# Optimization experiments

Hardware: AMD Instinct MI355X
Metric: run time of the kernel (lower is better)

Reference implementation:

```python
import jax, jax.numpy as jnp
import numpy as np
from jax import lax

N = 7  # patch size


def _conv3d(x, w, b):
    # x: [B,1,D,H,W], w: [1,1,3,3,3], b: [1]; VALID conv, stride 1
    y = lax.conv_general_dilated(x, w, (1, 1, 1), 'VALID',
                                 dimension_numbers=('NCDHW', 'OIDHW', 'NCDHW'))
    return y + b.reshape(1, -1, 1, 1, 1)


def _patches(x, k):
    # x: [B,1,D,H,W] -> [B*D'*H'*W', 1, k, k, k], row-major (kd,kh,kw) like torch unfold
    p = lax.conv_general_dilated_patches(x, (k, k, k), (1, 1, 1), 'VALID')
    # p: [B, k^3, D', H', W'] -> [B, D', H', W', k^3]
    p = jnp.transpose(p, (0, 2, 3, 4, 1))
    return p.reshape(-1, 1, k, k, k)


def setup_inputs() -> dict:
    key = jax.random.key(0)
    ks = jax.random.split(key, 12)
    inp = {
        'x': jax.random.normal(ks[0], (1, 1, 32, 128, 128), dtype=jnp.float32),
        'domain_neighbor': jax.random.uniform(ks[1], (1, 1, 9, 9, 9), dtype=jnp.float32),
        'guide_im': jax.random.normal(ks[2], (1, 1, 32, 128, 128), dtype=jnp.float32),
        # range coefficient conv stack (2 layers of Conv3d(1,1,3))
        'rw0': jax.random.normal(ks[3], (1, 1, 3, 3, 3), dtype=jnp.float32) * 0.3,
        'rb0': jnp.full((1,), 0.1, dtype=jnp.float32),
        'rw1': jax.random.normal(ks[4], (1, 1, 3, 3, 3), dtype=jnp.float32) * 0.3,
        'rb1': jnp.full((1,), 0.1, dtype=jnp.float32),
        # domain coefficient conv stack
        'dw0': jax.random.normal(ks[5], (1, 1, 3, 3, 3), dtype=jnp.float32) * 0.3,
        'db0': jnp.full((1,), 0.1, dtype=jnp.float32),
        'dw1': jax.random.normal(ks[6], (1, 1, 3, 3, 3), dtype=jnp.float32) * 0.3,
        'db1': jnp.full((1,), 0.1, dtype=jnp.float32),
    }
    return inp


def reference(x, domain_neighbor, guide_im, rw0, rb0, rw1, rb1, dw0, db0, dw1, db1):
    n = N
    c = n // 2
    # ---- range kernel: per-patch |guide - center|, then tiny conv stack ----
    g = _patches(guide_im, n)                     # [P,1,n,n,n]
    g = jnp.abs(g - g[:, :, c, c, c][:, :, None, None, None])
    rk = jax.nn.relu(_conv3d(g, rw0, rb0))
    rk = jax.nn.relu(_conv3d(rk, rw1, rb1))       # [P,1,3,3,3]
    # ---- domain kernel: center crop of distance kernel, same conv stack ----
    M = domain_neighbor.shape[2]
    cx = M // 2 - c
    dn = domain_neighbor[:, :, cx:cx + n, cx:cx + n, cx:cx + n]  # [1,1,n,n,n]
    dk = jax.nn.relu(_conv3d(dn, dw0, db0))
    dk = jax.nn.relu(_conv3d(dk, dw1, db1))       # [1,1,3,3,3]
    weights = dk * rk + 1e-10                     # [P,1,3,3,3]
    # ---- weighted average over 3x3x3 neighborhood of truncated x ----
    p = (n - 3) // 2
    xt = x[:, :, p:x.shape[2] - p, p:x.shape[3] - p, p:x.shape[4] - p]
    xu = _patches(xt, 3)                          # [P,1,3,3,3]
    num = jnp.sum(xu * weights, axis=(2, 3, 4))   # [P,1]
    den = jnp.sum(weights, axis=(2, 3, 4))        # [P,1]
    out = num / den
    B = x.shape[0]
    return out.reshape(B, 1, x.shape[2] - n + 1, x.shape[3] - n + 1, x.shape[4] - n + 1)
```

## Files before the change

kernel.cpp:

```cpp
#include <hip/hip_runtime.h>

#define OD 26
#define OH 122
#define OW 122
#define GS (128*128)
#define NOUT (OD*OH*OW)

#define TLX 14
#define TLY 14
#define TLZ 10
#define TLSLICE (TLX*TLY)
#define TLN (TLSLICE*TLZ)

__global__ void compute_dk_kernel(const float* __restrict__ dn,
                                  const float* __restrict__ dw0, const float* __restrict__ db0,
                                  const float* __restrict__ dw1, const float* __restrict__ db1,
                                  float* __restrict__ dk_out) {
    __shared__ float d0[125];
    int t = threadIdx.x;
    if (t < 125) {
        int tz = t / 25, ty = (t / 5) % 5, tx = t % 5;
        float acc = db0[0];
        #pragma unroll
        for (int kz = 0; kz < 3; ++kz)
            #pragma unroll
            for (int ky = 0; ky < 3; ++ky)
                #pragma unroll
                for (int kx = 0; kx < 3; ++kx)
                    acc += dw0[kz*9 + ky*3 + kx] *
                           dn[(1+tz+kz)*81 + (1+ty+ky)*9 + (1+tx+kx)];
        d0[t] = fmaxf(acc, 0.0f);
    }
    __syncthreads();
    if (t < 27) {
        int rz = t / 9, ry = (t / 3) % 3, rx = t % 3;
        float acc = db1[0];
        #pragma unroll
        for (int kz = 0; kz < 3; ++kz)
            #pragma unroll
            for (int ky = 0; ky < 3; ++ky)
                #pragma unroll
                for (int kx = 0; kx < 3; ++kx)
                    acc += dw1[kz*9 + ky*3 + kx] * d0[(rz+kz)*25 + (ry+ky)*5 + (rx+kx)];
        dk_out[t] = fmaxf(acc, 0.0f);
    }
}

__global__ __launch_bounds__(256) void jbf_main_kernel(
        const float* __restrict__ x, const float* __restrict__ guide,
        const float* __restrict__ rw0p, const float* __restrict__ rb0p,
        const float* __restrict__ rw1p, const float* __restrict__ rb1p,
        const float* __restrict__ dkp, float* __restrict__ out) {
    __shared__ float gl[TLN];

    const int xb = blockIdx.x * 8;
    const int yb = blockIdx.y * 8;
    const int zb = blockIdx.z * 4;

    for (int i = threadIdx.x; i < TLN; i += 256) {
        const int gx = i % TLX;
        const int gy = (i / TLX) % TLY;
        const int gz = i / TLSLICE;
        const int sx = min(xb + gx, 127);
        const int sy = min(yb + gy, 127);
        const int sz = min(zb + gz, 31);
        gl[i] = guide[sz*GS + sy*128 + sx];
    }
    __syncthreads();

    const int tx = threadIdx.x & 7;
    const int ty = (threadIdx.x >> 3) & 7;
    const int tz = threadIdx.x >> 6;
    const int x0 = xb + tx;
    const int y0 = yb + ty;
    const int z0 = zb + tz;
    if (x0 >= OW || y0 >= OH || z0 >= OD) return;

    float rw0[27], rw1[27];
    #pragma unroll
    for (int i = 0; i < 27; ++i) { rw0[i] = rw0p[i]; rw1[i] = rw1p[i]; }
    const float rb0 = rb0p[0], rb1 = rb1p[0];

    const float* glb = &gl[tz*TLSLICE + ty*TLX + tx];
    const float gc = glb[3*TLSLICE + 3*TLX + 3];

    float t0[125];
    #pragma unroll
    for (int i = 0; i < 125; ++i) t0[i] = rb0;

    #pragma unroll
    for (int gz = 0; gz < 7; ++gz) {
        #pragma unroll
        for (int gy = 0; gy < 7; ++gy) {
            float s[7];
            #pragma unroll
            for (int j = 0; j < 7; ++j)
                s[j] = glb[gz*TLSLICE + gy*TLX + j] - gc;
            #pragma unroll
            for (int kz = 0; kz < 3; ++kz) {
                const int tz1 = gz - kz;
                if (tz1 < 0 || tz1 > 4) continue;
                #pragma unroll
                for (int ky = 0; ky < 3; ++ky) {
                    const int ty1 = gy - ky;
                    if (ty1 < 0 || ty1 > 4) continue;
                    #pragma unroll
                    for (int txx = 0; txx < 5; ++txx)
                        #pragma unroll
                        for (int kx = 0; kx < 3; ++kx)
                            t0[tz1*25 + ty1*5 + txx] =
                                fmaf(rw0[kz*9 + ky*3 + kx], fabsf(s[txx + kx]),
                                     t0[tz1*25 + ty1*5 + txx]);
                }
            }
        }
    }
    #pragma unroll
    for (int i = 0; i < 125; ++i) t0[i] = fmaxf(t0[i], 0.0f);

    float num = 0.0f, den = 0.0f;
    const float* xbp = x + (z0+2)*GS + (y0+2)*128 + (x0+2);
    #pragma unroll
    for (int rz = 0; rz < 3; ++rz)
        #pragma unroll
        for (int ry = 0; ry < 3; ++ry)
            #pragma unroll
            for (int rx = 0; rx < 3; ++rx) {
                float acc = rb1;
                #pragma unroll
                for (int kz = 0; kz < 3; ++kz)
                    #pragma unroll
                    for (int ky = 0; ky < 3; ++ky)
                        #pragma unroll
                        for (int kx = 0; kx < 3; ++kx)
                            acc = fmaf(rw1[kz*9 + ky*3 + kx],
                                       t0[(rz+kz)*25 + (ry+ky)*5 + (rx+kx)], acc);
                const float w = dkp[rz*9 + ry*3 + rx] * fmaxf(acc, 0.0f) + 1e-10f;
                den += w;
                num = fmaf(w, xbp[rz*GS + ry*128 + rx], num);
            }

    out[(z0*OH + y0)*OW + x0] = num / den;
}

extern "C" void kernel_launch(void* const* d_in, const int* in_sizes, int n_in,
                              void* d_out, int out_size, void* d_ws, size_t ws_size,
                              hipStream_t stream) {
    const float* x     = (const float*)d_in[0];
    const float* dn    = (const float*)d_in[1];
    const float* guide = (const float*)d_in[2];
    const float* rw0   = (const float*)d_in[3];
    const float* rb0   = (const float*)d_in[4];
    const float* rw1   = (const float*)d_in[5];
    const float* rb1   = (const float*)d_in[6];
    const float* dw0   = (const float*)d_in[7];
    const float* db0   = (const float*)d_in[8];
    const float* dw1   = (const float*)d_in[9];
    const float* db1   = (const float*)d_in[10];
    float* out = (float*)d_out;
    float* dk  = (float*)d_ws;

    compute_dk_kernel<<<1, 128, 0, stream>>>(dn, dw0, db0, dw1, db1, dk);

    dim3 grid((OW + 7) / 8, (OH + 7) / 8, (OD + 3) / 4);
    jbf_main_kernel<<<grid, 256, 0, stream>>>(x, guide, rw0, rb0, rw1, rb1, dk, out);
}
```

Baseline: 149.4 us.

## Stream first conv layer per z-slice and fold second conv incrementally to cut registers

Restructures the per-thread two-layer conv so the 125-element intermediate is computed one 5x5 z-slice at a time and immediately accumulated into the 27 second-layer outputs, shrinking live register state from about 125 floats to 25+27. Adds launch_bounds min-blocks 3 to push occupancy and widens the shared tile row pitch from 14 to 20, likely to change bank mapping. The guide slices are reloaded from LDS per kz, raising LDS traffic, and the asm memory barrier limits compiler scheduling across slices.

```diff
diff --git a/kernel.cpp b/kernel.cpp
--- a/kernel.cpp
+++ b/kernel.cpp
@@ -6,7 +6,7 @@
 #define GS (128*128)
 #define NOUT (OD*OH*OW)
 
-#define TLX 14
+#define TLX 20
 #define TLY 14
 #define TLZ 10
 #define TLSLICE (TLX*TLY)
@@ -46,7 +46,7 @@
     }
 }
 
-__global__ __launch_bounds__(256) void jbf_main_kernel(
+__global__ __launch_bounds__(256, 3) void jbf_main_kernel(
         const float* __restrict__ x, const float* __restrict__ guide,
         const float* __restrict__ rw0p, const float* __restrict__ rb0p,
         const float* __restrict__ rw1p, const float* __restrict__ rb1p,
@@ -84,22 +84,25 @@
     const float* glb = &gl[tz*TLSLICE + ty*TLX + tx];
     const float gc = glb[3*TLSLICE + 3*TLX + 3];
 
-    float t0[125];
+    float rk[27];
     #pragma unroll
-    for (int i = 0; i < 125; ++i) t0[i] = rb0;
+    for (int i = 0; i < 27; ++i) rk[i] = rb1;
 
     #pragma unroll
-    for (int gz = 0; gz < 7; ++gz) {
+    for (int tz1 = 0; tz1 < 5; ++tz1) {
+        float t0s[25];
         #pragma unroll
-        for (int gy = 0; gy < 7; ++gy) {
-            float s[7];
+        for (int i = 0; i < 25; ++i) t0s[i] = rb0;
+
+        #pragma unroll
+        for (int kz = 0; kz < 3; ++kz) {
+            const int gz = tz1 + kz;
             #pragma unroll
-            for (int j = 0; j < 7; ++j)
-                s[j] = glb[gz*TLSLICE + gy*TLX + j] - gc;
-            #pragma unroll
-            for (int kz = 0; kz < 3; ++kz) {
-                const int tz1 = gz - kz;
-                if (tz1 < 0 || tz1 > 4) continue;
+            for (int gy = 0; gy < 7; ++gy) {
+                float s[7];
+                #pragma unroll
+                for (int j = 0; j < 7; ++j)
+                    s[j] = glb[gz*TLSLICE + gy*TLX + j] - gc;
                 #pragma unroll
                 for (int ky = 0; ky < 3; ++ky) {
                     const int ty1 = gy - ky;
@@ -108,15 +111,36 @@
                     for (int txx = 0; txx < 5; ++txx)
                         #pragma unroll
                         for (int kx = 0; kx < 3; ++kx)
-                            t0[tz1*25 + ty1*5 + txx] =
+                            t0s[ty1*5 + txx] =
                                 fmaf(rw0[kz*9 + ky*3 + kx], fabsf(s[txx + kx]),
-                                     t0[tz1*25 + ty1*5 + txx]);
+                                     t0s[ty1*5 + txx]);
                 }
             }
         }
+        #pragma unroll
+        for (int i = 0; i < 25; ++i) t0s[i] = fmaxf(t0s[i], 0.0f);
+
+        #pragma unroll
+        for (int kz2 = 0; kz2 < 3; ++kz2) {
+            const int rz = tz1 - kz2;
+            if (rz < 0 || rz > 2) continue;
+            #pragma unroll
+            for (int ry = 0; ry < 3; ++ry)
+                #pragma unroll
+                for (int rx = 0; rx < 3; ++rx) {
+                    #pragma unroll
+                    for (int ky2 = 0; ky2 < 3; ++ky2)
+                        #pragma unroll
+                        for (int kx2 = 0; kx2 < 3; ++kx2)
+                            rk[rz*9 + ry*3 + rx] =
+                                fmaf(rw1[kz2*9 + ky2*3 + kx2],
+                                     t0s[(ry+ky2)*5 + (rx+kx2)],
+                                     rk[rz*9 + ry*3 + rx]);
+                }
+        }
+
+        asm volatile("" ::: "memory");
     }
-    #pragma unroll
-    for (int i = 0; i < 125; ++i) t0[i] = fmaxf(t0[i], 0.0f);
 
     float num = 0.0f, den = 0.0f;
     const float* xbp = x + (z0+2)*GS + (y0+2)*128 + (x0+2);
@@ -126,16 +150,8 @@
         for (int ry = 0; ry < 3; ++ry)
             #pragma unroll
             for (int rx = 0; rx < 3; ++rx) {
-                float acc = rb1;
-                #pragma unroll
-                for (int kz = 0; kz < 3; ++kz)
-                    #pragma unroll
-                    for (int ky = 0; ky < 3; ++ky)
-                        #pragma unroll
-                        for (int kx = 0; kx < 3; ++kx)
-                            acc = fmaf(rw1[kz*9 + ky*3 + kx],
-                                       t0[(rz+kz)*25 + (ry+ky)*5 + (rx+kx)], acc);
-                const float w = dkp[rz*9 + ry*3 + rx] * fmaxf(acc, 0.0f) + 1e-10f;
+                const float w = dkp[rz*9 + ry*3 + rx]
+                              * fmaxf(rk[rz*9 + ry*3 + rx], 0.0f) + 1e-10f;
                 den += w;
                 num = fmaf(w, xbp[rz*GS + ry*128 + rx], num);
             }
```

Result: no change. 147.1 us (-1.6%).
